# Optimization experiments

Measured on AMD Instinct MI355X. Metric: run time of the kernel, lower is better.

## Reference

```python
import jax, jax.numpy as jnp
import numpy as np

PERIODS = (7, 30, 90)
KEEP_ORIGINAL = True
DROP_NA = False
T, F = 262144, 64


def setup_inputs() -> dict:
    key = jax.random.key(0)
    x = jax.random.normal(key, (T, F), dtype=jnp.float32)
    return {"x": x}


def _moving_average(x, cumsum, period):
    # drop_na=False path of _compute_ma:
    #   i <  period-1 : cumsum[i] / (i+1)   (i==0 gives x[0], same as cumsum[0]/1)
    #   i >= period-1 : (cumsum[i] - cumsum[i-period]) / period, with cumsum[i-period]=0 at i==period-1
    t = x.shape[0]
    idx = jnp.arange(t)
    shifted = jnp.concatenate(
        [jnp.zeros((period,) + x.shape[1:], dtype=x.dtype), cumsum[:-period]], axis=0
    )
    windowed = (cumsum - shifted) / jnp.asarray(period, x.dtype)
    expanding = cumsum / (idx + 1).astype(x.dtype)[:, None]
    return jnp.where((idx >= period - 1)[:, None], windowed, expanding)


def reference(x):
    cumsum = jnp.cumsum(x, axis=0)  # shared prefix sum across all periods
    parts = [x] if KEEP_ORIGINAL else []
    for p in PERIODS:
        parts.append(_moving_average(x, cumsum, p))
    # drop_na=False -> all parts have length T, min_batch_size = T
    return jnp.concatenate(parts, axis=-1)  # [T, (1+len(PERIODS))*F]
```

## Files before the change

kernel.cpp:

```cpp
#include <hip/hip_runtime.h>


#define T_ROWS 262144
#define F_COLS 64
#define OUT_COLS 256
#define TILE 128
#define HALO 90
#define STAGE_ROWS (TILE + HALO)
#define THREADS 512
#define STRIPS 8
#define STRIP_ROWS (TILE / STRIPS)

__global__ __launch_bounds__(THREADS) void ma_kernel(const float* __restrict__ x,
                                                     float* __restrict__ out) {
    __shared__ float lds[STAGE_ROWS * F_COLS];

    const int tid = threadIdx.x;
    const long base = (long)blockIdx.x * TILE;

    {
        const long g0f = (base - HALO) * F_COLS;
        float4* lds4 = (float4*)lds;
        const int n4 = STAGE_ROWS * F_COLS / 4;
        if (base >= HALO) {
            const float4* __restrict__ src = (const float4*)(x + g0f);
            for (int idx = tid; idx < n4; idx += THREADS)
                lds4[idx] = src[idx];
        } else {
            for (int idx = tid; idx < n4; idx += THREADS) {
                long gf = g0f + (long)idx * 4;
                float4 v = make_float4(0.f, 0.f, 0.f, 0.f);
                if (gf >= 0) v = *(const float4*)(x + gf);
                lds4[idx] = v;
            }
        }
    }
    __syncthreads();

    const int col   = tid & 63;
    const int strip = tid >> 6;
    const int lr0   = HALO + strip * STRIP_ROWS;
    const long g0   = base + strip * STRIP_ROWS;

    const float* __restrict__ lc = lds + col;

    float s7 = 0.f, s30 = 0.f, s90 = 0.f;
    #pragma unroll
    for (int k = 1; k <= 7; ++k)  s7  += lc[(lr0 - k) * F_COLS];
    s30 = s7;
    #pragma unroll
    for (int k = 8; k <= 30; ++k) s30 += lc[(lr0 - k) * F_COLS];
    s90 = s30;
    #pragma unroll
    for (int k = 31; k <= 90; ++k) s90 += lc[(lr0 - k) * F_COLS];

    float* __restrict__ oc = out + col;

    if (g0 < 89) {
        for (int j = 0; j < STRIP_ROWS; ++j) {
            const int lr = lr0 + j;
            const long gi = g0 + j;
            float v   = lc[lr * F_COLS];
            float o7  = lc[(lr - 7)  * F_COLS];
            float o30 = lc[(lr - 30) * F_COLS];
            float o90 = lc[(lr - 90) * F_COLS];
            s7 += v - o7; s30 += v - o30; s90 += v - o90;
            float fi  = (float)(gi + 1);
            float d7  = (gi < 6)  ? fi : 7.f;
            float d30 = (gi < 29) ? fi : 30.f;
            float d90 = (gi < 89) ? fi : 90.f;
            float* o = oc + gi * OUT_COLS;
            o[0]   = v;
            o[64]  = s7  / d7;
            o[128] = s30 / d30;
            o[192] = s90 / d90;
        }
    } else {
        const float r7 = 1.f / 7.f, r30 = 1.f / 30.f, r90 = 1.f / 90.f;
        #pragma unroll
        for (int j = 0; j < STRIP_ROWS; ++j) {
            const int lr = lr0 + j;
            float v   = lc[lr * F_COLS];
            float o7  = lc[(lr - 7)  * F_COLS];
            float o30 = lc[(lr - 30) * F_COLS];
            float o90 = lc[(lr - 90) * F_COLS];
            s7 += v - o7; s30 += v - o30; s90 += v - o90;
            float* o = oc + (g0 + j) * OUT_COLS;
            o[0]   = v;
            o[64]  = s7  * r7;
            o[128] = s30 * r30;
            o[192] = s90 * r90;
        }
    }
}

extern "C" void kernel_launch(void* const* d_in, const int* in_sizes, int n_in,
                              void* d_out, int out_size, void* d_ws, size_t ws_size,
                              hipStream_t stream) {
    const float* x = (const float*)d_in[0];
    float* out = (float*)d_out;
    const int n_blocks = T_ROWS / TILE;
    ma_kernel<<<n_blocks, THREADS, 0, stream>>>(x, out);
}
```

Baseline: 312.7 us.

## Process four tiles per block with an LDS ring buffer to reuse halo rows

Each block now walks four consecutive 128-row tiles, keeping rows in a 256-row LDS ring buffer so the 90-row halo is loaded once per block rather than once per tile. This cuts redundant global reads, which were about 70% extra input traffic. In exchange there are fewer blocks (512), the loads for each tile are serialized behind syncthreads with no overlap, and every LDS index needs extra masking.

```diff
diff --git a/kernel.cpp b/kernel.cpp
--- a/kernel.cpp
+++ b/kernel.cpp
@@ -6,90 +6,110 @@
 #define OUT_COLS 256
 #define TILE 128
 #define HALO 90
-#define STAGE_ROWS (TILE + HALO)
+#define NT 4
+#define BLOCK_ROWS (TILE * NT)
+#define RING 256
+#define RMASK (RING - 1)
 #define THREADS 512
 #define STRIPS 8
 #define STRIP_ROWS (TILE / STRIPS)
 
 __global__ __launch_bounds__(THREADS) void ma_kernel(const float* __restrict__ x,
                                                      float* __restrict__ out) {
-    __shared__ float lds[STAGE_ROWS * F_COLS];
+    __shared__ float lds[RING * F_COLS];
 
-    const int tid = threadIdx.x;
-    const long base = (long)blockIdx.x * TILE;
+    const int tid  = threadIdx.x;
+    const int base = blockIdx.x * BLOCK_ROWS;
 
-    {
-        const long g0f = (base - HALO) * F_COLS;
-        float4* lds4 = (float4*)lds;
-        const int n4 = STAGE_ROWS * F_COLS / 4;
-        if (base >= HALO) {
-            const float4* __restrict__ src = (const float4*)(x + g0f);
-            for (int idx = tid; idx < n4; idx += THREADS)
-                lds4[idx] = src[idx];
-        } else {
-            for (int idx = tid; idx < n4; idx += THREADS) {
-                long gf = g0f + (long)idx * 4;
-                float4 v = make_float4(0.f, 0.f, 0.f, 0.f);
-                if (gf >= 0) v = *(const float4*)(x + gf);
-                lds4[idx] = v;
-            }
+    float4* lds4 = (float4*)lds;
+    const float4* __restrict__ x4 = (const float4*)x;
+
+    if (base >= HALO) {
+        for (int idx = tid; idx < (HALO + TILE) * (F_COLS / 4); idx += THREADS) {
+            int r  = idx >> 4;
+            int c4 = idx & 15;
+            int gi = base - HALO + r;
+            lds4[(gi & RMASK) * 16 + c4] = x4[gi * 16 + c4];
+        }
+    } else {
+        for (int idx = tid; idx < (HALO + TILE) * (F_COLS / 4); idx += THREADS) {
+            int r  = idx >> 4;
+            int c4 = idx & 15;
+            int gi = base - HALO + r;
+            float4 v = make_float4(0.f, 0.f, 0.f, 0.f);
+            if (gi >= 0) v = x4[gi * 16 + c4];
+            lds4[(gi & RMASK) * 16 + c4] = v;
         }
     }
     __syncthreads();
 
     const int col   = tid & 63;
     const int strip = tid >> 6;
-    const int lr0   = HALO + strip * STRIP_ROWS;
-    const long g0   = base + strip * STRIP_ROWS;
+    const float* lc = lds + col;
+    float* oc = out + col;
+    const float r7 = 1.f / 7.f, r30 = 1.f / 30.f, r90 = 1.f / 90.f;
 
-    const float* __restrict__ lc = lds + col;
+    for (int t = 0; t < NT; ++t) {
+        const int g0  = base + t * TILE + strip * STRIP_ROWS;
+        const int lr0 = g0 & RMASK;
 
-    float s7 = 0.f, s30 = 0.f, s90 = 0.f;
-    #pragma unroll
-    for (int k = 1; k <= 7; ++k)  s7  += lc[(lr0 - k) * F_COLS];
-    s30 = s7;
-    #pragma unroll
-    for (int k = 8; k <= 30; ++k) s30 += lc[(lr0 - k) * F_COLS];
-    s90 = s30;
-    #pragma unroll
-    for (int k = 31; k <= 90; ++k) s90 += lc[(lr0 - k) * F_COLS];
+        float s7 = 0.f, s30 = 0.f, s90 = 0.f;
+        #pragma unroll
+        for (int k = 1; k <= 7; ++k)  s7  += lc[((lr0 - k) & RMASK) * F_COLS];
+        s30 = s7;
+        #pragma unroll
+        for (int k = 8; k <= 30; ++k) s30 += lc[((lr0 - k) & RMASK) * F_COLS];
+        s90 = s30;
+        #pragma unroll
+        for (int k = 31; k <= 90; ++k) s90 += lc[((lr0 - k) & RMASK) * F_COLS];
 
-    float* __restrict__ oc = out + col;
+        if (g0 < 89) {
+            for (int j = 0; j < STRIP_ROWS; ++j) {
+                int gi = g0 + j;
+                int lr = gi & RMASK;
+                float v   = lc[lr * F_COLS];
+                float o7  = lc[((lr - 7)  & RMASK) * F_COLS];
+                float o30 = lc[((lr - 30) & RMASK) * F_COLS];
+                float o90 = lc[((lr - 90) & RMASK) * F_COLS];
+                s7 += v - o7; s30 += v - o30; s90 += v - o90;
+                float fi  = (float)(gi + 1);
+                float d7  = (gi < 6)  ? fi : 7.f;
+                float d30 = (gi < 29) ? fi : 30.f;
+                float d90 = (gi < 89) ? fi : 90.f;
+                float* o = oc + gi * OUT_COLS;
+                o[0]   = v;
+                o[64]  = s7  / d7;
+                o[128] = s30 / d30;
+                o[192] = s90 / d90;
+            }
+        } else {
+            #pragma unroll
+            for (int j = 0; j < STRIP_ROWS; ++j) {
+                int gi = g0 + j;
+                int lr = gi & RMASK;
+                float v   = lc[lr * F_COLS];
+                float o7  = lc[((lr - 7)  & RMASK) * F_COLS];
+                float o30 = lc[((lr - 30) & RMASK) * F_COLS];
+                float o90 = lc[((lr - 90) & RMASK) * F_COLS];
+                s7 += v - o7; s30 += v - o30; s90 += v - o90;
+                float* o = oc + gi * OUT_COLS;
+                o[0]   = v;
+                o[64]  = s7  * r7;
+                o[128] = s30 * r30;
+                o[192] = s90 * r90;
+            }
+        }
 
-    if (g0 < 89) {
-        for (int j = 0; j < STRIP_ROWS; ++j) {
-            const int lr = lr0 + j;
-            const long gi = g0 + j;
-            float v   = lc[lr * F_COLS];
-            float o7  = lc[(lr - 7)  * F_COLS];
-            float o30 = lc[(lr - 30) * F_COLS];
-            float o90 = lc[(lr - 90) * F_COLS];
-            s7 += v - o7; s30 += v - o30; s90 += v - o90;
-            float fi  = (float)(gi + 1);
-            float d7  = (gi < 6)  ? fi : 7.f;
-            float d30 = (gi < 29) ? fi : 30.f;
-            float d90 = (gi < 89) ? fi : 90.f;
-            float* o = oc + gi * OUT_COLS;
-            o[0]   = v;
-            o[64]  = s7  / d7;
-            o[128] = s30 / d30;
-            o[192] = s90 / d90;
-        }
-    } else {
-        const float r7 = 1.f / 7.f, r30 = 1.f / 30.f, r90 = 1.f / 90.f;
-        #pragma unroll
-        for (int j = 0; j < STRIP_ROWS; ++j) {
-            const int lr = lr0 + j;
-            float v   = lc[lr * F_COLS];
-            float o7  = lc[(lr - 7)  * F_COLS];
-            float o30 = lc[(lr - 30) * F_COLS];
-            float o90 = lc[(lr - 90) * F_COLS];
-            s7 += v - o7; s30 += v - o30; s90 += v - o90;
-            float* o = oc + (g0 + j) * OUT_COLS;
-            o[0]   = v;
-            o[64]  = s7  * r7;
-            o[128] = s30 * r30;
-            o[192] = s90 * r90;
+        __syncthreads();
+        if (t + 1 < NT) {
+            const int nbase = base + (t + 1) * TILE;
+            for (int idx = tid; idx < TILE * (F_COLS / 4); idx += THREADS) {
+                int r  = idx >> 4;
+                int c4 = idx & 15;
+                int gi = nbase + r;
+                lds4[(gi & RMASK) * 16 + c4] = x4[gi * 16 + c4];
+            }
+            __syncthreads();
         }
     }
 }
@@ -99,6 +119,6 @@
                               hipStream_t stream) {
     const float* x = (const float*)d_in[0];
     float* out = (float*)d_out;
-    const int n_blocks = T_ROWS / TILE;
+    const int n_blocks = T_ROWS / BLOCK_ROWS;
     ma_kernel<<<n_blocks, THREADS, 0, stream>>>(x, out);
 }
```

After: 317.0 us. Within noise of the previous version (+1.4%).
